# Kernel tuning notes

Hardware: AMD Instinct MI355X
Metric: run time of the kernel (lower is better)

The kernel has to match this reference:

```python
import jax, jax.numpy as jnp
import numpy as np

DIM = 384
HEADS = 12
WH, WW = 7, 7
N = WH * WW
HEAD_DIM = DIM // HEADS
SCALE = HEAD_DIM ** -0.5


def _double_step_seq(step1, len1, step2, len2):
    seq1 = np.arange(0, step1 * len1, step1)
    seq2 = np.arange(0, step2 * len2, step2)
    return (seq1[:, None] + seq2[None, :]).reshape(1, -1)


def _rel_position_index():
    coords = _double_step_seq(2 * WW - 1, WH, 1, WW)  # (1, N)
    idx = coords + coords.T                            # (N, N)
    idx = idx[:, ::-1].copy()                          # flip along dim 1
    return jnp.asarray(idx, dtype=jnp.int32)

REL_IDX = _rel_position_index()


def setup_inputs() -> dict:
    key = jax.random.key(0)
    ks = jax.random.split(key, 6)
    B_ = 4096
    x = jax.random.normal(ks[0], (B_, N, DIM), dtype=jnp.float32)
    mask = jnp.zeros((64, N, N), dtype=jnp.float32)
    qkv_w = jax.random.normal(ks[1], (3 * DIM, DIM), dtype=jnp.float32) * 0.02
    qkv_b = jax.random.normal(ks[2], (3 * DIM,), dtype=jnp.float32) * 0.02
    proj_w = jax.random.normal(ks[3], (DIM, DIM), dtype=jnp.float32) * 0.02
    proj_b = jax.random.normal(ks[4], (DIM,), dtype=jnp.float32) * 0.02
    bias_table = jax.random.normal(ks[5], (169, HEADS), dtype=jnp.float32) * 0.02
    return {"x": x, "mask": mask, "qkv_w": qkv_w, "qkv_b": qkv_b,
            "proj_w": proj_w, "proj_b": proj_b, "bias_table": bias_table}


def reference(x, mask, qkv_w, qkv_b, proj_w, proj_b, bias_table):
    B_, n, C = x.shape
    # qkv projection: (B_, N, 3C) -> (3, B_, H, N, d)
    qkv = (x @ qkv_w.T + qkv_b).reshape(B_, n, 3, HEADS, HEAD_DIM)
    qkv = jnp.transpose(qkv, (2, 0, 3, 1, 4))
    q, k, v = qkv[0], qkv[1], qkv[2]
    q = q * SCALE
    attn = jnp.einsum('bhnd,bhmd->bhnm', q, k)  # (B_, H, N, N)
    # gathered relative position bias: (H, N, N)
    rel_bias = bias_table[REL_IDX.reshape(-1)].reshape(n, n, HEADS)
    rel_bias = jnp.transpose(rel_bias, (2, 0, 1))
    attn = attn + rel_bias[None]
    nW = mask.shape[0]
    attn = attn.reshape(B_ // nW, nW, HEADS, n, n) + mask[None, :, None]
    attn = attn.reshape(B_, HEADS, n, n)
    attn = jax.nn.softmax(attn, axis=-1)
    out = jnp.einsum('bhnm,bhmd->bnhd', attn, v).reshape(B_, n, C)
    out = out @ proj_w.T + proj_b
    return out
```

## Files before the change

### kernel.cpp

```cpp
#include <hip/hip_runtime.h>
#include <hip/hip_bf16.h>

#define NTOK 49
#define DIMC 384
#define NH 12
#define QSCALE 0.17677669529663687f

typedef __attribute__((ext_vector_type(8))) short short8;
typedef __attribute__((ext_vector_type(4))) float f32x4;
typedef unsigned int u32;

#define STG_OFF 0
#define KS_OFF  12288
#define VT_OFF  14336
#define PS_OFF  16384
#define QA_OFF  20480
#define BT_OFF  22528
#define QB_OFF  24556
#define SL_TOT  25708

#define NQFRAG (NH * 6 * 12)
#define WQB_SHORTS (NQFRAG * 512)
#define WPB_SHORTS (3 * 6 * 8192)
#define MB_TILES 1568
#define AV_BYTES ((size_t)MB_TILES * 6 * 16384)

__device__ __forceinline__ short f2bf(float f) {
    __bf16 h = (__bf16)f;
    return __builtin_bit_cast(short, h);
}
__device__ __forceinline__ float bf2f(short s) {
    u32 u = ((u32)(unsigned short)s) << 16;
    return __builtin_bit_cast(float, u);
}
__device__ __forceinline__ int cof(int p) { return 13 * (p / 7) + (p % 7); }

__device__ __forceinline__ void gld_lds16(const void* g, void* l) {
    __builtin_amdgcn_global_load_lds(
        (const __attribute__((address_space(1))) u32*)g,
        (__attribute__((address_space(3))) u32*)l, 16, 0, 0);
}

__device__ __forceinline__ short8 gather_bf(const float* __restrict__ w, int row, int k0) {
    const float* p = w + row * DIMC + k0;
    float4 a = *(const float4*)p;
    float4 b = *(const float4*)(p + 4);
    short8 r;
    r[0]=f2bf(a.x); r[1]=f2bf(a.y); r[2]=f2bf(a.z); r[3]=f2bf(a.w);
    r[4]=f2bf(b.x); r[5]=f2bf(b.y); r[6]=f2bf(b.z); r[7]=f2bf(b.w);
    return r;
}

__global__ void prep_weights(const float* __restrict__ qw, const float* __restrict__ pw,
                             short* __restrict__ wqb, short* __restrict__ wpb) {
    int gt = blockIdx.x * blockDim.x + threadIdx.x;
    if (gt < NQFRAG * 64) {
        int F = gt >> 6, lane = gt & 63;
        int h = F / 72, r = F % 72;
        int nt = r / 12, ks = r % 12;
        int l15 = lane & 15, l4 = lane >> 4;
        int grow = (nt >> 1) * DIMC + h * 32 + (nt & 1) * 16 + l15;
        const float* src = qw + grow * DIMC + ks * 32 + l4 * 8;
        short8 o;
        #pragma unroll
        for (int e = 0; e < 8; ++e) o[e] = f2bf(src[e]);
        *(short8*)(wqb + gt * 8) = o;
    } else if (gt < NQFRAG * 64 + 3 * 6 * 128 * 8) {
        int t2 = gt - NQFRAG * 64;
        int g  = t2 & 7;
        int r  = (t2 >> 3) & 127;
        int kc = (t2 >> 10) % 6;
        int nb = t2 / 6144;
        int k0 = kc * 64 + ((g ^ (r & 7)) << 3);
        const float* src = pw + (nb * 128 + r) * DIMC + k0;
        short8 o;
        #pragma unroll
        for (int e = 0; e < 8; ++e) o[e] = f2bf(src[e]);
        *(short8*)(wpb + (nb * 6 + kc) * 8192 + r * 64 + g * 8) = o;
    }
}

__global__ __launch_bounds__(256, 3)
void winattn_fused(const float* __restrict__ x, const float* __restrict__ mask,
                   const float* __restrict__ qkv_b, const float* __restrict__ bias_table,
                   const short* __restrict__ wqb, char* __restrict__ avb)
{
    __shared__ short SL[SL_TOT] __attribute__((aligned(128)));

    const int tid  = threadIdx.x;
    const int wv   = tid >> 6;
    const int lane = tid & 63;
    const int l15  = lane & 15;
    const int l4   = lane >> 4;
    const int win  = blockIdx.x;
    const int xbase = win * (NTOK * DIMC);

    for (int i = tid; i < 169 * NH; i += 256) SL[BT_OFF + i] = f2bf(bias_table[i]);
    for (int i = tid; i < 3 * DIMC; i += 256) SL[QB_OFF + i] = f2bf(qkv_b[i]);

    short8 xf[12];
    {
        const int row = wv * 16 + l15;
        const bool valid = row < NTOK;
        const float* xr = x + xbase + row * DIMC;
        #pragma unroll
        for (int ks = 0; ks < 12; ++ks) {
            short8 r;
            if (valid) {
                float4 a = *(const float4*)(xr + ks * 32 + l4 * 8);
                float4 b = *(const float4*)(xr + ks * 32 + l4 * 8 + 4);
                r[0]=f2bf(a.x); r[1]=f2bf(a.y); r[2]=f2bf(a.z); r[3]=f2bf(a.w);
                r[4]=f2bf(b.x); r[5]=f2bf(b.y); r[6]=f2bf(b.z); r[7]=f2bf(b.w);
            } else {
                r = (short8)0;
            }
            xf[ks] = r;
        }
    }

    float mv[4][4];
    int   bidx[4][4];
    float negm[4];
    {
        const float* maskp = mask + (win & 63) * (NTOK * NTOK);
        int cofi[4], cofm[4];
        #pragma unroll
        for (int t = 0; t < 4; ++t) {
            int m = t * 16 + l15;
            negm[t] = (m < NTOK) ? 0.f : -1e30f;
            int mm = m < NTOK ? m : 48;
            cofm[t] = cof(48 - mm);
            #pragma unroll
            for (int reg = 0; reg < 4; ++reg) {
                int i = wv * 16 + l4 * 4 + reg;
                mv[t][reg] = (i < NTOK && m < NTOK) ? maskp[i * NTOK + m] : 0.f;
            }
        }
        #pragma unroll
        for (int reg = 0; reg < 4; ++reg) {
            int i = wv * 16 + l4 * 4 + reg;
            cofi[reg] = cof(i < NTOK ? i : 48);
        }
        #pragma unroll
        for (int t = 0; t < 4; ++t)
            #pragma unroll
            for (int reg = 0; reg < 4; ++reg)
                bidx[t][reg] = (cofi[reg] + cofm[t]) * NH;
    }

    const f32x4 zf = (f32x4){0.f, 0.f, 0.f, 0.f};

    __syncthreads();

    #pragma unroll
    for (int t = 0; t < 3; ++t) {
        int j = wv * 3 + t;
        int F = (j >> 1) * 12 + (j & 1);
        gld_lds16(wqb + F * 512 + lane * 8, &SL[STG_OFF + j * 512]);
    }

    #pragma unroll 1
    for (int h = 0; h < NH; ++h) {
        f32x4 qa[6];
        #pragma unroll
        for (int nt = 0; nt < 6; ++nt) qa[nt] = zf;

        #pragma unroll
        for (int c = 0; c < 6; ++c) {
            __builtin_amdgcn_sched_barrier(0);
            asm volatile("s_waitcnt vmcnt(0)" ::: "memory");
            __builtin_amdgcn_s_barrier();
            __builtin_amdgcn_sched_barrier(0);
            {
                int hh = (c < 5) ? h : h + 1;
                int cc = (c < 5) ? c + 1 : 0;
                if (hh < NH) {
                    #pragma unroll
                    for (int t = 0; t < 3; ++t) {
                        int j = wv * 3 + t;
                        int F = (hh * 6 + (j >> 1)) * 12 + 2 * cc + (j & 1);
                        gld_lds16(wqb + F * 512 + lane * 8,
                                  &SL[STG_OFF + ((c + 1) & 1) * 6144 + j * 512]);
                    }
                }
            }
            __builtin_amdgcn_s_setprio(1);
            #pragma unroll
            for (int j = 0; j < 12; ++j) {
                short8 b = *(const short8*)&SL[STG_OFF + (c & 1) * 6144 + j * 512 + lane * 8];
                qa[j >> 1] = __builtin_amdgcn_mfma_f32_16x16x32_bf16(
                    xf[2 * c + (j & 1)], b, qa[j >> 1], 0, 0, 0);
            }
            __builtin_amdgcn_s_setprio(0);
        }

        #pragma unroll
        for (int nt = 0; nt < 6; ++nt) {
            const int sub = nt >> 1;
            const int colw = (nt & 1) * 16 + l15;
            const float bias = bf2f(SL[QB_OFF + sub * DIMC + h * 32 + colw]);
            #pragma unroll
            for (int reg = 0; reg < 4; ++reg) {
                const int tokg = wv * 16 + l4 * 4 + reg;
                float val = qa[nt][reg] + bias;
                if (sub == 0) {
                    int byt = tokg * 64 + (((colw << 1)) ^ ((tokg & 3) << 4));
                    SL[QA_OFF + (byt >> 1)] = f2bf(val * QSCALE);
                } else if (sub == 1) {
                    int byt = tokg * 64 + (((colw << 1)) ^ ((tokg & 3) << 4));
                    SL[KS_OFF + (byt >> 1)] = f2bf(val);
                } else {
                    int byt = colw * 128 + (((tokg << 1)) ^ ((colw & 7) << 4));
                    SL[VT_OFF + (byt >> 1)] = f2bf(val);
                }
            }
        }
        __syncthreads();

        short8 aq;
        {
            int row = wv * 16 + l15;
            int byt = row * 64 + ((l4 * 16) ^ ((row & 3) << 4));
            aq = *(const short8*)&SL[QA_OFF + (byt >> 1)];
        }
        f32x4 sc[4];
        #pragma unroll
        for (int t = 0; t < 4; ++t) {
            int row = t * 16 + l15;
            int byt = row * 64 + ((l4 * 16) ^ ((row & 3) << 4));
            short8 bk = *(const short8*)&SL[KS_OFF + (byt >> 1)];
            sc[t] = __builtin_amdgcn_mfma_f32_16x16x32_bf16(aq, bk, zf, 0, 0, 0);
        }
        float p[4][4];
        #pragma unroll
        for (int t = 0; t < 4; ++t) {
            #pragma unroll
            for (int reg = 0; reg < 4; ++reg) {
                float bt = bf2f(SL[BT_OFF + bidx[t][reg] + h]);
                p[t][reg] = sc[t][reg] + mv[t][reg] + bt + negm[t];
            }
        }
        #pragma unroll
        for (int reg = 0; reg < 4; ++reg) {
            float mx = fmaxf(fmaxf(p[0][reg], p[1][reg]), fmaxf(p[2][reg], p[3][reg]));
            #pragma unroll
            for (int off = 8; off >= 1; off >>= 1) mx = fmaxf(mx, __shfl_xor(mx, off, 64));
            float s0 = 0.f;
            #pragma unroll
            for (int t = 0; t < 4; ++t) { p[t][reg] = __expf(p[t][reg] - mx); s0 += p[t][reg]; }
            #pragma unroll
            for (int off = 8; off >= 1; off >>= 1) s0 += __shfl_xor(s0, off, 64);
            float rs = 1.f / s0;
            #pragma unroll
            for (int t = 0; t < 4; ++t) p[t][reg] *= rs;
        }
        #pragma unroll
        for (int t = 0; t < 4; ++t)
            #pragma unroll
            for (int reg = 0; reg < 4; ++reg) {
                int row = wv * 16 + l4 * 4 + reg;
                int byt = row * 128 + ((((t * 16 + l15) << 1)) ^ ((row & 7) << 4));
                SL[PS_OFF + (byt >> 1)] = f2bf(p[t][reg]);
            }

        f32x4 av[2];
        av[0] = zf; av[1] = zf;
        #pragma unroll
        for (int kst = 0; kst < 2; ++kst) {
            short8 pa;
            {
                int row = wv * 16 + l15;
                int byt = row * 128 + ((kst * 64 + l4 * 16) ^ ((row & 7) << 4));
                pa = *(const short8*)&SL[PS_OFF + (byt >> 1)];
            }
            #pragma unroll
            for (int dt = 0; dt < 2; ++dt) {
                int d = dt * 16 + l15;
                int byt = d * 128 + ((kst * 64 + l4 * 16) ^ ((d & 7) << 4));
                short8 bv = *(const short8*)&SL[VT_OFF + (byt >> 1)];
                av[dt] = __builtin_amdgcn_mfma_f32_16x16x32_bf16(pa, bv, av[dt], 0, 0, 0);
            }
        }
        #pragma unroll
        for (int dt = 0; dt < 2; ++dt)
            #pragma unroll
            for (int reg = 0; reg < 4; ++reg) {
                int tok = wv * 16 + l4 * 4 + reg;
                if (tok < NTOK) {
                    int gt = win * NTOK + tok;
                    int mb = gt >> 7, r = gt & 127;
                    int inner = ((((h & 1) << 6) | ((dt * 16 + l15) << 1))) ^ ((r & 7) << 4);
                    *(short*)(avb + (size_t)(mb * 6 + (h >> 1)) * 16384 + r * 128 + inner)
                        = f2bf(av[dt][reg]);
                }
            }
    }
}

__global__ __launch_bounds__(256, 2)
void proj_gemm(const char* __restrict__ avb, const short* __restrict__ wpb,
               const float* __restrict__ proj_b, float* __restrict__ out)
{
    __shared__ char LC[2][32768] __attribute__((aligned(128)));

    const int tid = threadIdx.x;
    const int wv = tid >> 6, lane = tid & 63;
    const int l15 = lane & 15, l4 = lane >> 4;
    const int wr = wv >> 1, wc = wv & 1;
    const int mb = blockIdx.x / 3, nb = blockIdx.x % 3;

    const char* asrc = avb + (size_t)mb * 6 * 16384;
    const char* bsrc = (const char*)wpb + (size_t)nb * 6 * 16384;

    f32x4 acc[4][4];
    #pragma unroll
    for (int mi = 0; mi < 4; ++mi)
        #pragma unroll
        for (int ni = 0; ni < 4; ++ni) acc[mi][ni] = (f32x4){0.f, 0.f, 0.f, 0.f};

    #pragma unroll
    for (int it = 0; it < 4; ++it) {
        int L = (wv * 4 + it) * 1024;
        gld_lds16(asrc + L + lane * 16, &LC[0][L]);
        gld_lds16(bsrc + L + lane * 16, &LC[0][16384 + L]);
    }

    #pragma unroll
    for (int kc = 0; kc < 6; ++kc) {
        __builtin_amdgcn_sched_barrier(0);
        asm volatile("s_waitcnt vmcnt(0)" ::: "memory");
        __builtin_amdgcn_s_barrier();
        __builtin_amdgcn_sched_barrier(0);
        if (kc < 5) {
            #pragma unroll
            for (int it = 0; it < 4; ++it) {
                int L = (wv * 4 + it) * 1024;
                gld_lds16(asrc + (kc + 1) * 16384 + L + lane * 16, &LC[(kc + 1) & 1][L]);
                gld_lds16(bsrc + (kc + 1) * 16384 + L + lane * 16, &LC[(kc + 1) & 1][16384 + L]);
            }
        }
        const char* bufp = LC[kc & 1];
        __builtin_amdgcn_s_setprio(1);
        #pragma unroll
        for (int ksub = 0; ksub < 2; ++ksub) {
            short8 a[4], b[4];
            #pragma unroll
            for (int mi = 0; mi < 4; ++mi) {
                int row = wr * 64 + mi * 16 + l15;
                a[mi] = *(const short8*)(bufp + row * 128 +
                        ((ksub * 64 + l4 * 16) ^ ((row & 7) << 4)));
            }
            #pragma unroll
            for (int ni = 0; ni < 4; ++ni) {
                int row = wc * 64 + ni * 16 + l15;
                b[ni] = *(const short8*)(bufp + 16384 + row * 128 +
                        ((ksub * 64 + l4 * 16) ^ ((row & 7) << 4)));
            }
            #pragma unroll
            for (int mi = 0; mi < 4; ++mi)
                #pragma unroll
                for (int ni = 0; ni < 4; ++ni)
                    acc[mi][ni] = __builtin_amdgcn_mfma_f32_16x16x32_bf16(
                        a[mi], b[ni], acc[mi][ni], 0, 0, 0);
        }
        __builtin_amdgcn_s_setprio(0);
    }

    float pb[4];
    #pragma unroll
    for (int ni = 0; ni < 4; ++ni) pb[ni] = proj_b[nb * 128 + wc * 64 + ni * 16 + l15];
    #pragma unroll
    for (int mi = 0; mi < 4; ++mi) {
        #pragma unroll
        for (int ni = 0; ni < 4; ++ni) {
            #pragma unroll
            for (int reg = 0; reg < 4; ++reg) {
                size_t row = (size_t)(mb * 128 + wr * 64 + mi * 16 + l4 * 4 + reg);
                out[row * DIMC + nb * 128 + wc * 64 + ni * 16 + l15] = acc[mi][ni][reg] + pb[ni];
            }
        }
    }
}

__global__ __launch_bounds__(256, 2)
void winattn_fallback(const float* __restrict__ x, const float* __restrict__ mask,
                      const float* __restrict__ qkv_w, const float* __restrict__ qkv_b,
                      const float* __restrict__ proj_w, const float* __restrict__ proj_b,
                      const float* __restrict__ bias_table, float* __restrict__ out)
{
    __shared__ short SL[SL_TOT] __attribute__((aligned(128)));
    const int tid = threadIdx.x, wv = tid >> 6, lane = tid & 63;
    const int l15 = lane & 15, l4 = lane >> 4;
    const int win = blockIdx.x;
    const int xbase = win * (NTOK * DIMC);

    short8 xf[12];
    {
        const int row = wv * 16 + l15;
        const bool valid = row < NTOK;
        const float* xr = x + xbase + row * DIMC;
        #pragma unroll
        for (int ks = 0; ks < 12; ++ks)
            xf[ks] = valid ? gather_bf(xr, 0, ks * 32 + l4 * 8) : (short8)0;
    }
    float mv[4][4]; int bidx[4][4]; float negm[4];
    {
        const float* maskp = mask + (win & 63) * (NTOK * NTOK);
        int cofi[4], cofm[4];
        #pragma unroll
        for (int t = 0; t < 4; ++t) {
            int m = t * 16 + l15;
            negm[t] = (m < NTOK) ? 0.f : -1e30f;
            cofm[t] = cof(48 - (m < NTOK ? m : 48));
            #pragma unroll
            for (int reg = 0; reg < 4; ++reg) {
                int i = wv * 16 + l4 * 4 + reg;
                mv[t][reg] = (i < NTOK && m < NTOK) ? maskp[i * NTOK + m] : 0.f;
            }
        }
        #pragma unroll
        for (int reg = 0; reg < 4; ++reg) {
            int i = wv * 16 + l4 * 4 + reg;
            cofi[reg] = cof(i < NTOK ? i : 48);
        }
        #pragma unroll
        for (int t = 0; t < 4; ++t)
            #pragma unroll
            for (int reg = 0; reg < 4; ++reg) bidx[t][reg] = (cofi[reg] + cofm[t]) * NH;
    }
    f32x4 pacc[24];
    #pragma unroll
    for (int t = 0; t < 24; ++t) pacc[t] = (f32x4){0.f, 0.f, 0.f, 0.f};
    const f32x4 zf = (f32x4){0.f, 0.f, 0.f, 0.f};
    __syncthreads();

    #pragma unroll 1
    for (int h = 0; h < NH; ++h) {
        f32x4 qa[6];
        #pragma unroll
        for (int nt = 0; nt < 6; ++nt) qa[nt] = zf;
        #pragma unroll
        for (int nt = 0; nt < 6; ++nt) {
            const int grow = (nt >> 1) * DIMC + h * 32 + (nt & 1) * 16 + l15;
            #pragma unroll
            for (int ks = 0; ks < 12; ++ks) {
                short8 b = gather_bf(qkv_w, grow, ks * 32 + l4 * 8);
                qa[nt] = __builtin_amdgcn_mfma_f32_16x16x32_bf16(xf[ks], b, qa[nt], 0, 0, 0);
            }
        }
        #pragma unroll
        for (int nt = 0; nt < 6; ++nt) {
            const int sub = nt >> 1;
            const int colw = (nt & 1) * 16 + l15;
            const float bias = qkv_b[sub * DIMC + h * 32 + colw];
            #pragma unroll
            for (int reg = 0; reg < 4; ++reg) {
                const int tokg = wv * 16 + l4 * 4 + reg;
                float val = qa[nt][reg] + bias;
                if (sub == 0) {
                    int byt = tokg * 64 + ((colw << 1) ^ ((tokg & 3) << 4));
                    SL[QA_OFF + (byt >> 1)] = f2bf(val * QSCALE);
                } else if (sub == 1) {
                    int byt = tokg * 64 + ((colw << 1) ^ ((tokg & 3) << 4));
                    SL[KS_OFF + (byt >> 1)] = f2bf(val);
                } else {
                    int byt = colw * 128 + ((tokg << 1) ^ ((colw & 7) << 4));
                    SL[VT_OFF + (byt >> 1)] = f2bf(val);
                }
            }
        }
        __syncthreads();
        short8 aq;
        { int row = wv*16+l15; int byt = row*64 + ((l4*16) ^ ((row&3)<<4));
          aq = *(const short8*)&SL[QA_OFF + (byt>>1)]; }
        f32x4 sc[4];
        #pragma unroll
        for (int t = 0; t < 4; ++t) {
            int row = t*16+l15; int byt = row*64 + ((l4*16) ^ ((row&3)<<4));
            short8 bk = *(const short8*)&SL[KS_OFF + (byt>>1)];
            sc[t] = __builtin_amdgcn_mfma_f32_16x16x32_bf16(aq, bk, zf, 0, 0, 0);
        }
        float p[4][4];
        #pragma unroll
        for (int t = 0; t < 4; ++t)
            #pragma unroll
            for (int reg = 0; reg < 4; ++reg)
                p[t][reg] = sc[t][reg] + mv[t][reg] + bias_table[bidx[t][reg] + h] + negm[t];
        #pragma unroll
        for (int reg = 0; reg < 4; ++reg) {
            float mx = fmaxf(fmaxf(p[0][reg], p[1][reg]), fmaxf(p[2][reg], p[3][reg]));
            #pragma unroll
            for (int off = 8; off >= 1; off >>= 1) mx = fmaxf(mx, __shfl_xor(mx, off, 64));
            float s0 = 0.f;
            #pragma unroll
            for (int t = 0; t < 4; ++t) { p[t][reg] = __expf(p[t][reg] - mx); s0 += p[t][reg]; }
            #pragma unroll
            for (int off = 8; off >= 1; off >>= 1) s0 += __shfl_xor(s0, off, 64);
            float rs = 1.f / s0;
            #pragma unroll
            for (int t = 0; t < 4; ++t) p[t][reg] *= rs;
        }
        #pragma unroll
        for (int t = 0; t < 4; ++t)
            #pragma unroll
            for (int reg = 0; reg < 4; ++reg) {
                int row = wv*16 + l4*4 + reg;
                int byt = row*128 + (((t*16+l15) << 1) ^ ((row&7)<<4));
                SL[PS_OFF + (byt>>1)] = f2bf(p[t][reg]);
            }
        f32x4 av[2]; av[0] = zf; av[1] = zf;
        #pragma unroll
        for (int kst = 0; kst < 2; ++kst) {
            short8 pa;
            { int row = wv*16+l15; int byt = row*128 + ((kst*64+l4*16) ^ ((row&7)<<4));
              pa = *(const short8*)&SL[PS_OFF + (byt>>1)]; }
            #pragma unroll
            for (int dt = 0; dt < 2; ++dt) {
                int d = dt*16+l15; int byt = d*128 + ((kst*64+l4*16) ^ ((d&7)<<4));
                short8 bv = *(const short8*)&SL[VT_OFF + (byt>>1)];
                av[dt] = __builtin_amdgcn_mfma_f32_16x16x32_bf16(pa, bv, av[dt], 0, 0, 0);
            }
        }
        __syncthreads();
        #pragma unroll
        for (int dt = 0; dt < 2; ++dt)
            #pragma unroll
            for (int reg = 0; reg < 4; ++reg) {
                int row = wv*16 + l4*4 + reg;
                int byt = row*64 + (((dt*16+l15) << 1) ^ ((row&3)<<4));
                SL[QA_OFF + (byt>>1)] = f2bf(av[dt][reg]);
            }
        __syncthreads();
        short8 aa;
        { int row = wv*16+l15; int byt = row*64 + ((l4*16) ^ ((row&3)<<4));
          aa = *(const short8*)&SL[QA_OFF + (byt>>1)]; }
        #pragma unroll
        for (int nt = 0; nt < 24; ++nt) {
            short8 bp = gather_bf(proj_w, nt * 16 + l15, h * 32 + l4 * 8);
            pacc[nt] = __builtin_amdgcn_mfma_f32_16x16x32_bf16(aa, bp, pacc[nt], 0, 0, 0);
        }
    }
    {
        float* op = out + xbase;
        #pragma unroll
        for (int nt = 0; nt < 24; ++nt) {
            const float pb = proj_b[nt * 16 + l15];
            #pragma unroll
            for (int reg = 0; reg < 4; ++reg) {
                const int i = wv * 16 + l4 * 4 + reg;
                if (i < NTOK) op[i * DIMC + nt * 16 + l15] = pacc[nt][reg] + pb;
            }
        }
    }
}

extern "C" void kernel_launch(void* const* d_in, const int* in_sizes, int n_in,
                              void* d_out, int out_size, void* d_ws, size_t ws_size,
                              hipStream_t stream) {
    const float* x          = (const float*)d_in[0];
    const float* mask       = (const float*)d_in[1];
    const float* qkv_w      = (const float*)d_in[2];
    const float* qkv_b      = (const float*)d_in[3];
    const float* proj_w     = (const float*)d_in[4];
    const float* proj_b     = (const float*)d_in[5];
    const float* bias_table = (const float*)d_in[6];
    float* out = (float*)d_out;

    const size_t need = (size_t)WQB_SHORTS * 2 + (size_t)WPB_SHORTS * 2 + AV_BYTES;
    if (ws_size >= need) {
        short* wqb = (short*)d_ws;
        short* wpb = wqb + WQB_SHORTS;
        char*  avb = (char*)(wpb + WPB_SHORTS);
        prep_weights<<<288, 256, 0, stream>>>(qkv_w, proj_w, wqb, wpb);
        winattn_fused<<<4096, 256, 0, stream>>>(x, mask, qkv_b, bias_table, wqb, avb);
        proj_gemm<<<MB_TILES * 3, 256, 0, stream>>>(avb, wpb, proj_b, out);
    } else {
        winattn_fallback<<<4096, 256, 0, stream>>>(x, mask, qkv_w, qkv_b, proj_w,
                                                   proj_b, bias_table, out);
    }
}
```

Before: 737.8 us.

## Process two windows per block, reusing staged QKV weight fragments across both

Each block now handles two windows, so every staged QKV weight fragment loaded into LDS feeds two MFMAs, which halves weight traffic per window. The staging ring grows from two to three buffers, and the wait becomes vmcnt(3) so two prefetches stay in flight. The mask and padding are precomputed and packed as bf16 pairs to save registers, and P and Q scratch become per-wave. Register and LDS use rise, so launch bounds drop to two blocks per CU, which lowers occupancy.

```diff
diff --git a/kernel.cpp b/kernel.cpp
--- a/kernel.cpp
+++ b/kernel.cpp
@@ -11,13 +11,13 @@
 typedef unsigned int u32;
 
 #define STG_OFF 0
-#define KS_OFF  12288
-#define VT_OFF  14336
-#define PS_OFF  16384
-#define QA_OFF  20480
-#define BT_OFF  22528
-#define QB_OFF  24556
-#define SL_TOT  25708
+#define KS_OFF  18432
+#define VT_OFF  22528
+#define PS_OFF  26624
+#define QA_OFF  30720
+#define BT_OFF  34816
+#define QB_OFF  36848
+#define SL_TOT  38000
 
 #define NQFRAG (NH * 6 * 12)
 #define WQB_SHORTS (NQFRAG * 512)
@@ -80,7 +80,7 @@
     }
 }
 
-__global__ __launch_bounds__(256, 3)
+__global__ __launch_bounds__(256, 2)
 void winattn_fused(const float* __restrict__ x, const float* __restrict__ mask,
                    const float* __restrict__ qkv_b, const float* __restrict__ bias_table,
                    const short* __restrict__ wqb, char* __restrict__ avb)
@@ -92,49 +92,62 @@
     const int lane = tid & 63;
     const int l15  = lane & 15;
     const int l4   = lane >> 4;
-    const int win  = blockIdx.x;
-    const int xbase = win * (NTOK * DIMC);
+    const int win0 = blockIdx.x * 2;
 
     for (int i = tid; i < 169 * NH; i += 256) SL[BT_OFF + i] = f2bf(bias_table[i]);
     for (int i = tid; i < 3 * DIMC; i += 256) SL[QB_OFF + i] = f2bf(qkv_b[i]);
 
-    short8 xf[12];
+    short8 xf0[12], xf1[12];
     {
         const int row = wv * 16 + l15;
         const bool valid = row < NTOK;
-        const float* xr = x + xbase + row * DIMC;
-        #pragma unroll
-        for (int ks = 0; ks < 12; ++ks) {
-            short8 r;
-            if (valid) {
-                float4 a = *(const float4*)(xr + ks * 32 + l4 * 8);
-                float4 b = *(const float4*)(xr + ks * 32 + l4 * 8 + 4);
-                r[0]=f2bf(a.x); r[1]=f2bf(a.y); r[2]=f2bf(a.z); r[3]=f2bf(a.w);
-                r[4]=f2bf(b.x); r[5]=f2bf(b.y); r[6]=f2bf(b.z); r[7]=f2bf(b.w);
-            } else {
-                r = (short8)0;
-            }
-            xf[ks] = r;
-        }
-    }
-
-    float mv[4][4];
-    int   bidx[4][4];
-    float negm[4];
+        #pragma unroll
+        for (int st = 0; st < 2; ++st) {
+            const float* xr = x + (size_t)(win0 + st) * (NTOK * DIMC) + row * DIMC;
+            #pragma unroll
+            for (int ks = 0; ks < 12; ++ks) {
+                short8 r;
+                if (valid) {
+                    float4 a = *(const float4*)(xr + ks * 32 + l4 * 8);
+                    float4 b = *(const float4*)(xr + ks * 32 + l4 * 8 + 4);
+                    r[0]=f2bf(a.x); r[1]=f2bf(a.y); r[2]=f2bf(a.z); r[3]=f2bf(a.w);
+                    r[4]=f2bf(b.x); r[5]=f2bf(b.y); r[6]=f2bf(b.z); r[7]=f2bf(b.w);
+                } else {
+                    r = (short8)0;
+                }
+                if (st == 0) xf0[ks] = r; else xf1[ks] = r;
+            }
+        }
+    }
+
+    u32 mvp[2][4][2];
+    int bidx[4][4];
     {
-        const float* maskp = mask + (win & 63) * (NTOK * NTOK);
+        #pragma unroll
+        for (int st = 0; st < 2; ++st) {
+            const float* maskp = mask + (size_t)((win0 + st) & 63) * (NTOK * NTOK);
+            #pragma unroll
+            for (int t = 0; t < 4; ++t) {
+                int m = t * 16 + l15;
+                float pad = (m < NTOK) ? 0.f : -1e30f;
+                #pragma unroll
+                for (int rp = 0; rp < 2; ++rp) {
+                    float v[2];
+                    #pragma unroll
+                    for (int e = 0; e < 2; ++e) {
+                        int i = wv * 16 + l4 * 4 + rp * 2 + e;
+                        v[e] = ((i < NTOK && m < NTOK) ? maskp[i * NTOK + m] : 0.f) + pad;
+                    }
+                    mvp[st][t][rp] = (u32)(unsigned short)f2bf(v[0]) |
+                                     ((u32)(unsigned short)f2bf(v[1]) << 16);
+                }
+            }
+        }
         int cofi[4], cofm[4];
         #pragma unroll
         for (int t = 0; t < 4; ++t) {
             int m = t * 16 + l15;
-            negm[t] = (m < NTOK) ? 0.f : -1e30f;
-            int mm = m < NTOK ? m : 48;
-            cofm[t] = cof(48 - mm);
-            #pragma unroll
-            for (int reg = 0; reg < 4; ++reg) {
-                int i = wv * 16 + l4 * 4 + reg;
-                mv[t][reg] = (i < NTOK && m < NTOK) ? maskp[i * NTOK + m] : 0.f;
-            }
+            cofm[t] = cof(48 - (m < NTOK ? m : 48));
         }
         #pragma unroll
         for (int reg = 0; reg < 4; ++reg) {
@@ -153,147 +166,159 @@
     __syncthreads();
 
     #pragma unroll
-    for (int t = 0; t < 3; ++t) {
-        int j = wv * 3 + t;
-        int F = (j >> 1) * 12 + (j & 1);
-        gld_lds16(wqb + F * 512 + lane * 8, &SL[STG_OFF + j * 512]);
+    for (int pc = 0; pc < 2; ++pc) {
+        #pragma unroll
+        for (int t = 0; t < 3; ++t) {
+            int jf = wv * 3 + t;
+            int F = (jf >> 1) * 12 + 2 * pc + (jf & 1);
+            gld_lds16(wqb + F * 512 + lane * 8, &SL[STG_OFF + pc * 6144 + jf * 512]);
+        }
     }
 
     #pragma unroll 1
     for (int h = 0; h < NH; ++h) {
-        f32x4 qa[6];
-        #pragma unroll
-        for (int nt = 0; nt < 6; ++nt) qa[nt] = zf;
+        f32x4 qa[12];
+        #pragma unroll
+        for (int t = 0; t < 12; ++t) qa[t] = zf;
 
         #pragma unroll
         for (int c = 0; c < 6; ++c) {
-            __builtin_amdgcn_sched_barrier(0);
-            asm volatile("s_waitcnt vmcnt(0)" ::: "memory");
+            asm volatile("s_waitcnt vmcnt(3)" ::: "memory");
             __builtin_amdgcn_s_barrier();
             __builtin_amdgcn_sched_barrier(0);
             {
-                int hh = (c < 5) ? h : h + 1;
-                int cc = (c < 5) ? c + 1 : 0;
-                if (hh < NH) {
-                    #pragma unroll
-                    for (int t = 0; t < 3; ++t) {
-                        int j = wv * 3 + t;
-                        int F = (hh * 6 + (j >> 1)) * 12 + 2 * cc + (j & 1);
-                        gld_lds16(wqb + F * 512 + lane * 8,
-                                  &SL[STG_OFF + ((c + 1) & 1) * 6144 + j * 512]);
+                int cg2 = h * 6 + c + 2;
+                if (cg2 >= 72) cg2 -= 72;
+                int hh = cg2 / 6, cc = cg2 - hh * 6;
+                #pragma unroll
+                for (int t = 0; t < 3; ++t) {
+                    int jf = wv * 3 + t;
+                    int F = (hh * 6 + (jf >> 1)) * 12 + 2 * cc + (jf & 1);
+                    gld_lds16(wqb + F * 512 + lane * 8,
+                              &SL[STG_OFF + ((c + 2) % 3) * 6144 + jf * 512]);
+                }
+            }
+            __builtin_amdgcn_sched_barrier(0);
+            const short* buf = &SL[STG_OFF + (c % 3) * 6144];
+            __builtin_amdgcn_s_setprio(1);
+            #pragma unroll
+            for (int j = 0; j < 12; ++j) {
+                short8 b = *(const short8*)(buf + j * 512 + lane * 8);
+                const int nt = j >> 1, kk = 2 * c + (j & 1);
+                qa[nt]     = __builtin_amdgcn_mfma_f32_16x16x32_bf16(xf0[kk], b, qa[nt], 0, 0, 0);
+                qa[6 + nt] = __builtin_amdgcn_mfma_f32_16x16x32_bf16(xf1[kk], b, qa[6 + nt], 0, 0, 0);
+            }
+            __builtin_amdgcn_s_setprio(0);
+        }
+
+        #pragma unroll
+        for (int st = 0; st < 2; ++st) {
+            #pragma unroll
+            for (int nt = 0; nt < 6; ++nt) {
+                const int sub = nt >> 1;
+                const int colw = (nt & 1) * 16 + l15;
+                const float bias = bf2f(SL[QB_OFF + sub * DIMC + h * 32 + colw]);
+                #pragma unroll
+                for (int reg = 0; reg < 4; ++reg) {
+                    const int rl = l4 * 4 + reg;
+                    const int tokg = wv * 16 + rl;
+                    float val = qa[st * 6 + nt][reg] + bias;
+                    if (sub == 0) {
+                        int byt = rl * 64 + ((colw << 1) ^ ((rl & 3) << 4));
+                        SL[QA_OFF + (wv * 2 + st) * 512 + (byt >> 1)] = f2bf(val * QSCALE);
+                    } else if (sub == 1) {
+                        int byt = tokg * 64 + ((colw << 1) ^ ((tokg & 3) << 4));
+                        SL[KS_OFF + st * 2048 + (byt >> 1)] = f2bf(val);
+                    } else {
+                        int byt = colw * 128 + ((tokg << 1) ^ ((colw & 7) << 4));
+                        SL[VT_OFF + st * 2048 + (byt >> 1)] = f2bf(val);
                     }
                 }
             }
-            __builtin_amdgcn_s_setprio(1);
-            #pragma unroll
-            for (int j = 0; j < 12; ++j) {
-                short8 b = *(const short8*)&SL[STG_OFF + (c & 1) * 6144 + j * 512 + lane * 8];
-                qa[j >> 1] = __builtin_amdgcn_mfma_f32_16x16x32_bf16(
-                    xf[2 * c + (j & 1)], b, qa[j >> 1], 0, 0, 0);
-            }
-            __builtin_amdgcn_s_setprio(0);
-        }
-
-        #pragma unroll
-        for (int nt = 0; nt < 6; ++nt) {
-            const int sub = nt >> 1;
-            const int colw = (nt & 1) * 16 + l15;
-            const float bias = bf2f(SL[QB_OFF + sub * DIMC + h * 32 + colw]);
+        }
+        asm volatile("s_waitcnt lgkmcnt(0)" ::: "memory");
+        __builtin_amdgcn_s_barrier();
+        __builtin_amdgcn_sched_barrier(0);
+
+        #pragma unroll
+        for (int st = 0; st < 2; ++st) {
+            short8 aq;
+            {
+                int byt = l15 * 64 + ((l4 * 16) ^ ((l15 & 3) << 4));
+                aq = *(const short8*)&SL[QA_OFF + (wv * 2 + st) * 512 + (byt >> 1)];
+            }
+            f32x4 sc[4];
+            #pragma unroll
+            for (int t = 0; t < 4; ++t) {
+                int row = t * 16 + l15;
+                int byt = row * 64 + ((l4 * 16) ^ ((row & 3) << 4));
+                short8 bk = *(const short8*)&SL[KS_OFF + st * 2048 + (byt >> 1)];
+                sc[t] = __builtin_amdgcn_mfma_f32_16x16x32_bf16(aq, bk, zf, 0, 0, 0);
+            }
+            float p[4][4];
+            #pragma unroll
+            for (int t = 0; t < 4; ++t) {
+                #pragma unroll
+                for (int reg = 0; reg < 4; ++reg) {
+                    u32 pk = mvp[st][t][reg >> 1];
+                    float mval = bf2f((short)((reg & 1) ? (pk >> 16) : (pk & 0xffff)));
+                    float bt = bf2f(SL[BT_OFF + bidx[t][reg] + h]);
+                    p[t][reg] = sc[t][reg] + mval + bt;
+                }
+            }
             #pragma unroll
             for (int reg = 0; reg < 4; ++reg) {
-                const int tokg = wv * 16 + l4 * 4 + reg;
-                float val = qa[nt][reg] + bias;
-                if (sub == 0) {
-                    int byt = tokg * 64 + (((colw << 1)) ^ ((tokg & 3) << 4));
-                    SL[QA_OFF + (byt >> 1)] = f2bf(val * QSCALE);
-                } else if (sub == 1) {
-                    int byt = tokg * 64 + (((colw << 1)) ^ ((tokg & 3) << 4));
-                    SL[KS_OFF + (byt >> 1)] = f2bf(val);
-                } else {
-                    int byt = colw * 128 + (((tokg << 1)) ^ ((colw & 7) << 4));
-                    SL[VT_OFF + (byt >> 1)] = f2bf(val);
-                }
-            }
-        }
-        __syncthreads();
-
-        short8 aq;
-        {
-            int row = wv * 16 + l15;
-            int byt = row * 64 + ((l4 * 16) ^ ((row & 3) << 4));
-            aq = *(const short8*)&SL[QA_OFF + (byt >> 1)];
-        }
-        f32x4 sc[4];
-        #pragma unroll
-        for (int t = 0; t < 4; ++t) {
-            int row = t * 16 + l15;
-            int byt = row * 64 + ((l4 * 16) ^ ((row & 3) << 4));
-            short8 bk = *(const short8*)&SL[KS_OFF + (byt >> 1)];
-            sc[t] = __builtin_amdgcn_mfma_f32_16x16x32_bf16(aq, bk, zf, 0, 0, 0);
-        }
-        float p[4][4];
-        #pragma unroll
-        for (int t = 0; t < 4; ++t) {
-            #pragma unroll
-            for (int reg = 0; reg < 4; ++reg) {
-                float bt = bf2f(SL[BT_OFF + bidx[t][reg] + h]);
-                p[t][reg] = sc[t][reg] + mv[t][reg] + bt + negm[t];
-            }
-        }
-        #pragma unroll
-        for (int reg = 0; reg < 4; ++reg) {
-            float mx = fmaxf(fmaxf(p[0][reg], p[1][reg]), fmaxf(p[2][reg], p[3][reg]));
-            #pragma unroll
-            for (int off = 8; off >= 1; off >>= 1) mx = fmaxf(mx, __shfl_xor(mx, off, 64));
-            float s0 = 0.f;
-            #pragma unroll
-            for (int t = 0; t < 4; ++t) { p[t][reg] = __expf(p[t][reg] - mx); s0 += p[t][reg]; }
-            #pragma unroll
-            for (int off = 8; off >= 1; off >>= 1) s0 += __shfl_xor(s0, off, 64);
-            float rs = 1.f / s0;
-            #pragma unroll
-            for (int t = 0; t < 4; ++t) p[t][reg] *= rs;
-        }
-        #pragma unroll
-        for (int t = 0; t < 4; ++t)
-            #pragma unroll
-            for (int reg = 0; reg < 4; ++reg) {
-                int row = wv * 16 + l4 * 4 + reg;
-                int byt = row * 128 + ((((t * 16 + l15) << 1)) ^ ((row & 7) << 4));
-                SL[PS_OFF + (byt >> 1)] = f2bf(p[t][reg]);
-            }
-
-        f32x4 av[2];
-        av[0] = zf; av[1] = zf;
-        #pragma unroll
-        for (int kst = 0; kst < 2; ++kst) {
-            short8 pa;
-            {
-                int row = wv * 16 + l15;
-                int byt = row * 128 + ((kst * 64 + l4 * 16) ^ ((row & 7) << 4));
-                pa = *(const short8*)&SL[PS_OFF + (byt >> 1)];
-            }
-            #pragma unroll
-            for (int dt = 0; dt < 2; ++dt) {
-                int d = dt * 16 + l15;
-                int byt = d * 128 + ((kst * 64 + l4 * 16) ^ ((d & 7) << 4));
-                short8 bv = *(const short8*)&SL[VT_OFF + (byt >> 1)];
-                av[dt] = __builtin_amdgcn_mfma_f32_16x16x32_bf16(pa, bv, av[dt], 0, 0, 0);
-            }
-        }
-        #pragma unroll
-        for (int dt = 0; dt < 2; ++dt)
-            #pragma unroll
-            for (int reg = 0; reg < 4; ++reg) {
-                int tok = wv * 16 + l4 * 4 + reg;
-                if (tok < NTOK) {
-                    int gt = win * NTOK + tok;
-                    int mb = gt >> 7, r = gt & 127;
-                    int inner = ((((h & 1) << 6) | ((dt * 16 + l15) << 1))) ^ ((r & 7) << 4);
-                    *(short*)(avb + (size_t)(mb * 6 + (h >> 1)) * 16384 + r * 128 + inner)
-                        = f2bf(av[dt][reg]);
-                }
-            }
+                float mx = fmaxf(fmaxf(p[0][reg], p[1][reg]), fmaxf(p[2][reg], p[3][reg]));
+                #pragma unroll
+                for (int off = 8; off >= 1; off >>= 1) mx = fmaxf(mx, __shfl_xor(mx, off, 64));
+                float s0 = 0.f;
+                #pragma unroll
+                for (int t = 0; t < 4; ++t) { p[t][reg] = __expf(p[t][reg] - mx); s0 += p[t][reg]; }
+                #pragma unroll
+                for (int off = 8; off >= 1; off >>= 1) s0 += __shfl_xor(s0, off, 64);
+                float rs = 1.f / s0;
+                #pragma unroll
+                for (int t = 0; t < 4; ++t) p[t][reg] *= rs;
+            }
+            #pragma unroll
+            for (int t = 0; t < 4; ++t)
+                #pragma unroll
+                for (int reg = 0; reg < 4; ++reg) {
+                    int r = l4 * 4 + reg;
+                    int byt = r * 128 + ((((t * 16 + l15) << 1)) ^ ((r & 7) << 4));
+                    SL[PS_OFF + wv * 1024 + (byt >> 1)] = f2bf(p[t][reg]);
+                }
+            f32x4 av[2];
+            av[0] = zf; av[1] = zf;
+            #pragma unroll
+            for (int kst = 0; kst < 2; ++kst) {
+                short8 pa;
+                {
+                    int byt = l15 * 128 + (((kst * 64 + l4 * 16)) ^ ((l15 & 7) << 4));
+                    pa = *(const short8*)&SL[PS_OFF + wv * 1024 + (byt >> 1)];
+                }
+                #pragma unroll
+                for (int dt = 0; dt < 2; ++dt) {
+                    int d = dt * 16 + l15;
+                    int byt = d * 128 + (((kst * 64 + l4 * 16)) ^ ((d & 7) << 4));
+                    short8 bv = *(const short8*)&SL[VT_OFF + st * 2048 + (byt >> 1)];
+                    av[dt] = __builtin_amdgcn_mfma_f32_16x16x32_bf16(pa, bv, av[dt], 0, 0, 0);
+                }
+            }
+            #pragma unroll
+            for (int dt = 0; dt < 2; ++dt)
+                #pragma unroll
+                for (int reg = 0; reg < 4; ++reg) {
+                    int tok = wv * 16 + l4 * 4 + reg;
+                    if (tok < NTOK) {
+                        int gt = (win0 + st) * NTOK + tok;
+                        int mb = gt >> 7, r = gt & 127;
+                        int inner = ((((h & 1) << 6) | ((dt * 16 + l15) << 1))) ^ ((r & 7) << 4);
+                        *(short*)(avb + (size_t)(mb * 6 + (h >> 1)) * 16384 + r * 128 + inner)
+                            = f2bf(av[dt][reg]);
+                    }
+                }
+        }
     }
 }
 
@@ -388,11 +413,12 @@
                       const float* __restrict__ proj_w, const float* __restrict__ proj_b,
                       const float* __restrict__ bias_table, float* __restrict__ out)
 {
-    __shared__ short SL[SL_TOT] __attribute__((aligned(128)));
+    __shared__ short SL[26624] __attribute__((aligned(128)));
     const int tid = threadIdx.x, wv = tid >> 6, lane = tid & 63;
     const int l15 = lane & 15, l4 = lane >> 4;
     const int win = blockIdx.x;
     const int xbase = win * (NTOK * DIMC);
+    const int KSo = 0, VTo = 2048, PSo = 4096, QAo = 8192;
 
     short8 xf[12];
     {
@@ -459,25 +485,25 @@
                 float val = qa[nt][reg] + bias;
                 if (sub == 0) {
                     int byt = tokg * 64 + ((colw << 1) ^ ((tokg & 3) << 4));
-                    SL[QA_OFF + (byt >> 1)] = f2bf(val * QSCALE);
+                    SL[QAo + (byt >> 1)] = f2bf(val * QSCALE);
                 } else if (sub == 1) {
                     int byt = tokg * 64 + ((colw << 1) ^ ((tokg & 3) << 4));
-                    SL[KS_OFF + (byt >> 1)] = f2bf(val);
+                    SL[KSo + (byt >> 1)] = f2bf(val);
                 } else {
                     int byt = colw * 128 + ((tokg << 1) ^ ((colw & 7) << 4));
-                    SL[VT_OFF + (byt >> 1)] = f2bf(val);
+                    SL[VTo + (byt >> 1)] = f2bf(val);
                 }
             }
         }
         __syncthreads();
         short8 aq;
         { int row = wv*16+l15; int byt = row*64 + ((l4*16) ^ ((row&3)<<4));
-          aq = *(const short8*)&SL[QA_OFF + (byt>>1)]; }
+          aq = *(const short8*)&SL[QAo + (byt>>1)]; }
         f32x4 sc[4];
         #pragma unroll
         for (int t = 0; t < 4; ++t) {
             int row = t*16+l15; int byt = row*64 + ((l4*16) ^ ((row&3)<<4));
-            short8 bk = *(const short8*)&SL[KS_OFF + (byt>>1)];
+            short8 bk = *(const short8*)&SL[KSo + (byt>>1)];
             sc[t] = __builtin_amdgcn_mfma_f32_16x16x32_bf16(aq, bk, zf, 0, 0, 0);
         }
         float p[4][4];
@@ -506,18 +532,18 @@
             for (int reg = 0; reg < 4; ++reg) {
                 int row = wv*16 + l4*4 + reg;
                 int byt = row*128 + (((t*16+l15) << 1) ^ ((row&7)<<4));
-                SL[PS_OFF + (byt>>1)] = f2bf(p[t][reg]);
+                SL[PSo + (byt>>1)] = f2bf(p[t][reg]);
             }
         f32x4 av[2]; av[0] = zf; av[1] = zf;
         #pragma unroll
         for (int kst = 0; kst < 2; ++kst) {
             short8 pa;
             { int row = wv*16+l15; int byt = row*128 + ((kst*64+l4*16) ^ ((row&7)<<4));
-              pa = *(const short8*)&SL[PS_OFF + (byt>>1)]; }
+              pa = *(const short8*)&SL[PSo + (byt>>1)]; }
             #pragma unroll
             for (int dt = 0; dt < 2; ++dt) {
                 int d = dt*16+l15; int byt = d*128 + ((kst*64+l4*16) ^ ((d&7)<<4));
-                short8 bv = *(const short8*)&SL[VT_OFF + (byt>>1)];
+                short8 bv = *(const short8*)&SL[VTo + (byt>>1)];
                 av[dt] = __builtin_amdgcn_mfma_f32_16x16x32_bf16(pa, bv, av[dt], 0, 0, 0);
             }
         }
@@ -528,12 +554,12 @@
             for (int reg = 0; reg < 4; ++reg) {
                 int row = wv*16 + l4*4 + reg;
                 int byt = row*64 + (((dt*16+l15) << 1) ^ ((row&3)<<4));
-                SL[QA_OFF + (byt>>1)] = f2bf(av[dt][reg]);
+                SL[QAo + (byt>>1)] = f2bf(av[dt][reg]);
             }
         __syncthreads();
         short8 aa;
         { int row = wv*16+l15; int byt = row*64 + ((l4*16) ^ ((row&3)<<4));
-          aa = *(const short8*)&SL[QA_OFF + (byt>>1)]; }
+          aa = *(const short8*)&SL[QAo + (byt>>1)]; }
         #pragma unroll
         for (int nt = 0; nt < 24; ++nt) {
             short8 bp = gather_bf(proj_w, nt * 16 + l15, h * 32 + l4 * 8);
@@ -572,7 +598,7 @@
         short* wpb = wqb + WQB_SHORTS;
         char*  avb = (char*)(wpb + WPB_SHORTS);
         prep_weights<<<288, 256, 0, stream>>>(qkv_w, proj_w, wqb, wpb);
-        winattn_fused<<<4096, 256, 0, stream>>>(x, mask, qkv_b, bias_table, wqb, avb);
+        winattn_fused<<<2048, 256, 0, stream>>>(x, mask, qkv_b, bias_table, wqb, avb);
         proj_gemm<<<MB_TILES * 3, 256, 0, stream>>>(avb, wpb, proj_b, out);
     } else {
         winattn_fallback<<<4096, 256, 0, stream>>>(x, mask, qkv_w, qkv_b, proj_w,
```

Result: slower. 871.4 us (+18.1%).
